# Performance work log

Hardware: AMD Instinct MI355X
Metric: run time of the kernel (lower is better)

The kernel has to match this reference:

```python
import jax, jax.numpy as jnp
import numpy as np

TAU = 0.1
NUM_HEADS = 8
HEAD_DIMS = 64


def setup_inputs() -> dict:
    key = jax.random.key(0)
    ks = jax.random.split(key, 5)
    B, T, D = 4, 1024, 512
    H, Dh = NUM_HEADS, HEAD_DIMS
    x = jax.random.normal(ks[0], (B, T, D), dtype=jnp.float32)
    scale = 1.0 / np.sqrt(D)
    wq = jax.random.normal(ks[1], (D, H * Dh), dtype=jnp.float32) * scale
    wk = jax.random.normal(ks[2], (D, H * Dh), dtype=jnp.float32) * scale
    wv = jax.random.normal(ks[3], (D, H * Dh), dtype=jnp.float32) * scale
    wo = jax.random.normal(ks[4], (H * Dh, D // H), dtype=jnp.float32) * scale
    return {"x": x, "wq": wq, "wk": wk, "wv": wv, "wo": wo}


def _scan_score(a, tau):
    # a: [B,H,T,T] soft-match scores; tau > 0 branch of _rosa_qkv_scan_score
    T = a.shape[-1]
    r = jnp.arange(T)
    future = r[:, None] < r[None, :]                       # [T,T], True above diag
    a = jnp.where(future[None, None], 0.0, a)
    # rotate columns: out[...,i,j] = a[...,i,(i+j+1) % T]
    c1 = (r[:, None] + r[None, :] + 1) % T                 # [T,T]
    a = jnp.take_along_axis(a, c1[None, None], axis=-1)
    cs = jnp.cumsum(a, axis=-2)                            # cumsum over rows i
    a = cs - jax.lax.cummax(cs * (1.0 - a), axis=2)        # run-length style scan
    # rotate back: out[...,i,j] = a[...,i,(j-i+T-1) % T]
    c2 = (r[None, :] - r[:, None] + T - 1) % T
    a = jnp.take_along_axis(a, c2[None, None], axis=-1)
    return a


def _attn_score(a, tau):
    # tau > 0 branch of _rosa_qkv_attn_score: positional tie-break + causal softmax
    T = a.shape[-1]
    r = jnp.arange(T)
    p = r.astype(a.dtype)
    pos = p[None, :] / (p[:, None] + 1.0)                  # p[i,j] = j/(i+1)
    future = r[:, None] < r[None, :]
    a = jnp.where(future[None, None], -jnp.inf, a + pos[None, None])
    return jax.nn.softmax(a / tau, axis=-1)


def reference(x, wq, wk, wv, wo):
    B, T, D = x.shape
    H, Dh = NUM_HEADS, HEAD_DIMS
    tau = TAU
    iq = (x @ wq).reshape(B, T, H, Dh)
    ik = (x @ wk).reshape(B, T, H, Dh)
    iv = (x @ wv).reshape(B, T, H, Dh)
    iq_sm = jax.nn.softmax(iq / tau, axis=-1).astype(jnp.float32)
    ik_sm = jax.nn.softmax(ik / tau, axis=-1).astype(jnp.float32)
    iv_sm = jax.nn.softmax(iv / tau, axis=-1).astype(jnp.float32)
    # match scores [B,H,T,T]
    a = jnp.einsum("bihd,bjhd->bhij", iq_sm, ik_sm)
    a = _scan_score(a, tau)
    a = _attn_score(a, tau)
    o = jnp.einsum("bhij,bjhd->bhid", a, iv_sm)            # [B,H,T,Dh]
    xv = wo.reshape(H, Dh, D // H)
    o = jnp.einsum("bhid,hde->bhie", o, xv)                # [B,H,T,D//H]
    return o.transpose(0, 2, 1, 3).reshape(B, T, D)
```

## Files before the change

### kernel.cpp

```cpp
#include <hip/hip_runtime.h>
#include <math.h>

#define BB    4
#define TT    1024
#define DD    512
#define NH    8
#define DH    64
#define BH    32
#define INV_TAU 10.0f

typedef __attribute__((ext_vector_type(8))) short short8;
typedef __attribute__((ext_vector_type(4))) float f4;
typedef __attribute__((ext_vector_type(8))) _Float16 half8;

__device__ inline unsigned short f2bf(float f) {
  unsigned u = __float_as_uint(f);
  u += 0x7FFFu + ((u >> 16) & 1u);
  return (unsigned short)(u >> 16);
}
__device__ inline float bf2f(unsigned short h) {
  return __uint_as_float(((unsigned)h) << 16);
}
__device__ inline unsigned short f2bf_t(float f) {
  return (unsigned short)(__float_as_uint(f) >> 16);
}

__global__ __launch_bounds__(256) void k_prep(
    const float* __restrict__ x, const float* __restrict__ wq,
    const float* __restrict__ wk, const float* __restrict__ wv,
    unsigned short* __restrict__ xh, unsigned short* __restrict__ xl,
    unsigned short* __restrict__ wth, unsigned short* __restrict__ wtl)
{
  __shared__ float Wf[64][65];
  const int blk = blockIdx.x;
  const int tid = threadIdx.x;
  if (blk < 2048) {
    const int i = (blk * 256 + tid) * 4;
    float4 v = *(const float4*)&x[i];
    ushort4 h, l;
    h.x = f2bf_t(v.x); l.x = f2bf_t(v.x - bf2f(h.x));
    h.y = f2bf_t(v.y); l.y = f2bf_t(v.y - bf2f(h.y));
    h.z = f2bf_t(v.z); l.z = f2bf_t(v.z - bf2f(h.z));
    h.w = f2bf_t(v.w); l.w = f2bf_t(v.w - bf2f(h.w));
    *(ushort4*)&xh[i] = h;
    *(ushort4*)&xl[i] = l;
    return;
  }
  const int b = blk - 2048;
  const int ten = b >> 6;
  const int r = b & 63;
  const int n0 = (r & 7) * 64, k0 = (r >> 3) * 64;
  const float* W = (ten == 0) ? wq : ((ten == 1) ? wk : wv);
#pragma unroll
  for (int p = 0; p < 4; ++p) {
    int kk = p * 16 + (tid >> 4);
    int nn = (tid & 15) * 4;
    float4 v = *(const float4*)&W[(size_t)(k0 + kk) * 512 + n0 + nn];
    Wf[kk][nn + 0] = v.x; Wf[kk][nn + 1] = v.y;
    Wf[kk][nn + 2] = v.z; Wf[kk][nn + 3] = v.w;
  }
  __syncthreads();
  const int n = tid >> 2, kq = tid & 3;
  size_t base = ((size_t)(ten * 512 + n0 + n)) * 512 + k0 + kq * 16;
#pragma unroll
  for (int jj = 0; jj < 4; ++jj) {
    ushort4 h, l;
    float f0 = Wf[kq * 16 + jj * 4 + 0][n];
    float f1 = Wf[kq * 16 + jj * 4 + 1][n];
    float f2 = Wf[kq * 16 + jj * 4 + 2][n];
    float f3 = Wf[kq * 16 + jj * 4 + 3][n];
    h.x = f2bf_t(f0); l.x = f2bf_t(f0 - bf2f(h.x));
    h.y = f2bf_t(f1); l.y = f2bf_t(f1 - bf2f(h.y));
    h.z = f2bf_t(f2); l.z = f2bf_t(f2 - bf2f(h.z));
    h.w = f2bf_t(f3); l.w = f2bf_t(f3 - bf2f(h.w));
    *(ushort4*)&wth[base + jj * 4] = h;
    *(ushort4*)&wtl[base + jj * 4] = l;
  }
}

__global__ __launch_bounds__(256) void k_proj_mfma(
    const unsigned short* __restrict__ xh, const unsigned short* __restrict__ xl,
    const unsigned short* __restrict__ wth, const unsigned short* __restrict__ wtl,
    unsigned short* __restrict__ qh, unsigned short* __restrict__ ql,
    unsigned short* __restrict__ kh, unsigned short* __restrict__ kl,
    float* __restrict__ vs)
{
  __shared__ unsigned short Ah[64][40];
  __shared__ unsigned short Al[64][40];
  __shared__ unsigned short Bh[128][40];
  __shared__ unsigned short Bl[128][40];
  const int tid = threadIdx.x;
  const int n0g = blockIdx.x * 128;
  const int m0 = blockIdx.y * 64;
  const int w = tid >> 6, lane = tid & 63;
  const int mw = (w & 1) * 32, nw = (w >> 1) * 64;
  const int quad = lane >> 4, l16 = lane & 15;
  const int srow = tid >> 2;
  const int sk = (tid & 3) * 8;

  f4 acc[2][4] = {};

  for (int k0 = 0; k0 < DD; k0 += 32) {
    short8 a0 = *(const short8*)&xh[(size_t)(m0 + srow) * DD + k0 + sk];
    short8 a1 = *(const short8*)&xl[(size_t)(m0 + srow) * DD + k0 + sk];
    short8 b0 = *(const short8*)&wth[(size_t)(n0g + srow) * DD + k0 + sk];
    short8 b1 = *(const short8*)&wth[(size_t)(n0g + 64 + srow) * DD + k0 + sk];
    short8 b2 = *(const short8*)&wtl[(size_t)(n0g + srow) * DD + k0 + sk];
    short8 b3 = *(const short8*)&wtl[(size_t)(n0g + 64 + srow) * DD + k0 + sk];
    *(short8*)&Ah[srow][sk] = a0;
    *(short8*)&Al[srow][sk] = a1;
    *(short8*)&Bh[srow][sk] = b0;  *(short8*)&Bh[64 + srow][sk] = b1;
    *(short8*)&Bl[srow][sk] = b2;  *(short8*)&Bl[64 + srow][sk] = b3;
    __syncthreads();

    short8 fbh[4], fbl[4];
#pragma unroll
    for (int nt = 0; nt < 4; ++nt) {
      fbh[nt] = *(const short8*)&Bh[nw + nt * 16 + l16][quad * 8];
      fbl[nt] = *(const short8*)&Bl[nw + nt * 16 + l16][quad * 8];
    }
#pragma unroll
    for (int mt = 0; mt < 2; ++mt) {
      short8 fah = *(const short8*)&Ah[mw + mt * 16 + l16][quad * 8];
      short8 fal = *(const short8*)&Al[mw + mt * 16 + l16][quad * 8];
#pragma unroll
      for (int nt = 0; nt < 4; ++nt) {
        acc[mt][nt] = __builtin_amdgcn_mfma_f32_16x16x32_bf16(fah, fbh[nt], acc[mt][nt], 0, 0, 0);
        acc[mt][nt] = __builtin_amdgcn_mfma_f32_16x16x32_bf16(fah, fbl[nt], acc[mt][nt], 0, 0, 0);
        acc[mt][nt] = __builtin_amdgcn_mfma_f32_16x16x32_bf16(fal, fbh[nt], acc[mt][nt], 0, 0, 0);
      }
    }
    __syncthreads();
  }

  const int tensor = n0g >> 9;
  const int ncol = (n0g & 511) + nw;
  const int h = ncol >> 6;
#pragma unroll
  for (int mt = 0; mt < 2; ++mt) {
#pragma unroll
    for (int r = 0; r < 4; ++r) {
      float v0 = acc[mt][0][r], v1 = acc[mt][1][r];
      float v2 = acc[mt][2][r], v3 = acc[mt][3][r];
      float mx = fmaxf(fmaxf(v0, v1), fmaxf(v2, v3));
#pragma unroll
      for (int msk = 1; msk <= 8; msk <<= 1) mx = fmaxf(mx, __shfl_xor(mx, msk, 64));
      float e0 = __expf((v0 - mx) * INV_TAU);
      float e1 = __expf((v1 - mx) * INV_TAU);
      float e2 = __expf((v2 - mx) * INV_TAU);
      float e3 = __expf((v3 - mx) * INV_TAU);
      float sm = e0 + e1 + e2 + e3;
#pragma unroll
      for (int msk = 1; msk <= 8; msk <<= 1) sm += __shfl_xor(sm, msk, 64);
      float inv = 1.0f / sm;
      int row = m0 + mw + mt * 16 + quad * 4 + r;
      int b = row >> 10, t = row & 1023;
      size_t base = (((size_t)b * NH + h) * TT + t) * DH;
      float e[4] = {e0 * inv, e1 * inv, e2 * inv, e3 * inv};
      if (tensor == 2) {
#pragma unroll
        for (int c = 0; c < 4; ++c) vs[base + l16 + c * 16] = e[c];
      } else {
        unsigned short* oh = tensor ? kh : qh;
        unsigned short* ol = tensor ? kl : ql;
#pragma unroll
        for (int c = 0; c < 4; ++c) {
          unsigned short hh = f2bf_t(e[c]);
          oh[base + l16 + c * 16] = hh;
          ol[base + l16 + c * 16] = f2bf_t(e[c] - bf2f(hh));
        }
      }
    }
  }
}

__global__ __launch_bounds__(256) void k_qkv(
    const unsigned short* __restrict__ qh, const unsigned short* __restrict__ ql,
    const unsigned short* __restrict__ kh, const unsigned short* __restrict__ kl,
    _Float16* __restrict__ A, const float* __restrict__ vs,
    unsigned short* __restrict__ vth, unsigned short* __restrict__ vtl)
{
  __shared__ char smem[4][32][68 * 2];
  const int tid = threadIdx.x;
  if (blockIdx.x >= 1088) {
    float (*Vf)[65] = (float(*)[65])smem;
    const int b = blockIdx.x - 1088;
    const int z = b & 31, t0 = (b >> 5) * 64;
#pragma unroll
    for (int it = 0; it < 4; ++it) {
      int tl = it * 16 + (tid >> 4);
      int d4 = (tid & 15) * 4;
      float4 v = *(const float4*)&vs[((size_t)z * TT + t0 + tl) * DH + d4];
      Vf[tl][d4 + 0] = v.x; Vf[tl][d4 + 1] = v.y;
      Vf[tl][d4 + 2] = v.z; Vf[tl][d4 + 3] = v.w;
    }
    __syncthreads();
#pragma unroll
    for (int it = 0; it < 8; ++it) {
      int d = it * 8 + (tid >> 5);
      int t = (tid & 31) * 2;
      float a0 = Vf[t][d], a1 = Vf[t + 1][d];
      unsigned short h0 = f2bf_t(a0), h1 = f2bf_t(a1);
      unsigned short l0 = f2bf_t(a0 - bf2f(h0)), l1 = f2bf_t(a1 - bf2f(h1));
      size_t o = ((size_t)z * DH + d) * TT + t0 + t;
      ushort2 hh; hh.x = h0; hh.y = h1;
      ushort2 ll; ll.x = l0; ll.y = l1;
      *(ushort2*)&vth[o] = hh;
      *(ushort2*)&vtl[o] = ll;
    }
    return;
  }
  const int gid = blockIdx.x * 4 + (tid >> 6);
  const int z = gid / 136;
  const int lx = gid - z * 136;
  int ti = (int)((sqrtf(8.0f * lx + 1.0f) - 1.0f) * 0.5f);
  while ((ti + 1) * (ti + 2) / 2 <= lx) ++ti;
  while (ti * (ti + 1) / 2 > lx) --ti;
  const int tj = lx - ti * (ti + 1) / 2;
  const int i0 = ti * 64, j0 = tj * 64;
  const int w = tid >> 6;
  const int lane = tid & 63;
  const int quad = lane >> 4, l16 = lane & 15;
  const size_t zb = (size_t)z * TT * DH;

  short8 fbh[4][2], fbl[4][2];
#pragma unroll
  for (int nt = 0; nt < 4; ++nt)
#pragma unroll
    for (int ks = 0; ks < 2; ++ks) {
      size_t o = zb + (size_t)(j0 + nt * 16 + l16) * DH + ks * 32 + quad * 8;
      fbh[nt][ks] = *(const short8*)&kh[o];
      fbl[nt][ks] = *(const short8*)&kl[o];
    }

  f4 acc[4][4] = {};
#pragma unroll
  for (int mt = 0; mt < 4; ++mt) {
    short8 fah[2], fal[2];
#pragma unroll
    for (int ks = 0; ks < 2; ++ks) {
      size_t o = zb + (size_t)(i0 + mt * 16 + l16) * DH + ks * 32 + quad * 8;
      fah[ks] = *(const short8*)&qh[o];
      fal[ks] = *(const short8*)&ql[o];
    }
#pragma unroll
    for (int nt = 0; nt < 4; ++nt)
#pragma unroll
      for (int ks = 0; ks < 2; ++ks) {
        acc[mt][nt] = __builtin_amdgcn_mfma_f32_16x16x32_bf16(fah[ks], fbh[nt][ks], acc[mt][nt], 0, 0, 0);
        acc[mt][nt] = __builtin_amdgcn_mfma_f32_16x16x32_bf16(fah[ks], fbl[nt][ks], acc[mt][nt], 0, 0, 0);
        acc[mt][nt] = __builtin_amdgcn_mfma_f32_16x16x32_bf16(fal[ks], fbh[nt][ks], acc[mt][nt], 0, 0, 0);
      }
  }

  _Float16* Ab = A + (size_t)z * TT * TT;
  _Float16 (*Ts)[68] = (_Float16(*)[68])smem[w];
#pragma unroll
  for (int round = 0; round < 2; ++round) {
#pragma unroll
    for (int m2 = 0; m2 < 2; ++m2) {
      int mt = round * 2 + m2;
#pragma unroll
      for (int nt = 0; nt < 4; ++nt)
#pragma unroll
        for (int r = 0; r < 4; ++r)
          Ts[m2 * 16 + quad * 4 + r][nt * 16 + l16] = (_Float16)acc[mt][nt][r];
    }
    const int rrow = lane >> 3, seg = (lane & 7) * 8;
#pragma unroll
    for (int r2 = 0; r2 < 4; ++r2) {
      int row = rrow + 8 * r2;
      half8 v = *(const half8*)&Ts[row][seg];
      *(half8*)&Ab[(size_t)(i0 + round * 32 + row) * TT + j0 + seg] = v;
    }
  }
}

__global__ __launch_bounds__(1024) void k_scan(_Float16* __restrict__ A)
{
  __shared__ float Ssum[16][64];
  __shared__ float Gmax[16][64];
  const int blk = blockIdx.x;
  const int p = blk >> 5;
  const int xb = (p < 8) ? p : (23 - p);
  const int z = blk & 31;
  const int lane = threadIdx.x & 63;
  const int w = threadIdx.x >> 6;
  _Float16* __restrict__ Ab = A + (size_t)z * TT * TT;
  const int dbase = xb * 64;
  const int d = dbase + lane;
  const int L = (TT - dbase) >> 4;
  const int r0 = dbase + w * L;

  float S = 0.0f;
#pragma unroll 8
  for (int t = 0; t < L; ++t) {
    int i = r0 + t;
    size_t idx = (i >= d) ? ((size_t)i * (TT + 1) - d) : 0;
    float s = (float)Ab[idx];
    S += (i >= d) ? s : 0.0f;
  }
  Ssum[w][lane] = S;
  __syncthreads();

  float cs_in = 0.0f;
  for (int ww = 0; ww < w; ++ww) cs_in += Ssum[ww][lane];

  {
    float lcs = 0.0f, gm = 0.0f;
#pragma unroll 8
    for (int t = 0; t < L; ++t) {
      int i = r0 + t;
      size_t idx = (i >= d) ? ((size_t)i * (TT + 1) - d) : 0;
      float s0 = (float)Ab[idx];
      float s = (i >= d) ? s0 : 0.0f;
      lcs += s;
      gm = fmaxf(gm, (cs_in + lcs) * (1.0f - s));
    }
    Gmax[w][lane] = gm;
  }
  __syncthreads();

  float m = 0.0f;
  for (int ww = 0; ww < w; ++ww) m = fmaxf(m, Gmax[ww][lane]);

  {
    float lcs = 0.0f;
#pragma unroll 8
    for (int t = 0; t < L; ++t) {
      int i = r0 + t;
      bool ok = (i >= d);
      size_t idx = ok ? ((size_t)i * (TT + 1) - d) : 0;
      float s0 = (float)Ab[idx];
      float s = ok ? s0 : 0.0f;
      lcs += s;
      float cs = cs_in + lcs;
      m = fmaxf(m, cs * (1.0f - s));
      if (ok) Ab[idx] = (_Float16)(cs - m);
    }
  }
}

__global__ __launch_bounds__(64) void k_pv(
    const _Float16* __restrict__ A, const unsigned short* __restrict__ vth,
    const unsigned short* __restrict__ vtl, float* __restrict__ oatt,
    float* __restrict__ Opart, float* __restrict__ ml)
{
  const int lane = threadIdx.x;
  const int quad = lane >> 4, l16 = lane & 15;
  const int blk = blockIdx.x;
  const int z = blk & 31;
  const int item = blk >> 5;
  int ti, band, jt0, jt1, chunk;
  bool split;
  if (item < 32) {
    ti = 8 + (item >> 2); band = item & 3; jt0 = 0; jt1 = 8; chunk = 0; split = true;
  } else {
    int i2 = item - 32;
    int l = 8 - (i2 >> 3);
    int sub = i2 & 7;
    band = sub & 3;
    if (sub < 4) { ti = l + 7; jt0 = 8; jt1 = ti + 1; chunk = 1; split = true; }
    else         { ti = l - 1; jt0 = 0; jt1 = ti + 1; chunk = 0; split = false; }
  }
  const _Float16* Az = A + (size_t)z * TT * TT;
  const unsigned short* vh = vth + (size_t)z * DH * TT;
  const unsigned short* vl = vtl + (size_t)z * DH * TT;

  const int i0 = ti * 64;
  const int irow = i0 + band * 16 + l16;
  const float invi = 1.0f / (float)(irow + 1);
  f4 acc[4] = {};
  float m_old = -3e38f, l_run = 0.0f;

  float posu[16];
#pragma unroll
  for (int u = 0; u < 16; ++u)
    posu[u] = (float)((u >> 3) * 32 + quad * 8 + (u & 7)) * invi;
  const float jstep = 64.0f * invi;
  float jtoff = (float)jt0 * jstep;

  for (int jt = jt0; jt < jt1; ++jt) {
    const bool masked = (jt == ti);
    float sc[16];
#pragma unroll
    for (int ks = 0; ks < 2; ++ks) {
      half8 hv = *(const half8*)&Az[(size_t)irow * TT + jt * 64 + ks * 32 + quad * 8];
#pragma unroll
      for (int u = 0; u < 8; ++u) sc[ks * 8 + u] = (float)hv[u];
    }
#pragma unroll
    for (int u = 0; u < 16; ++u) {
      float v = sc[u] + (jtoff + posu[u]);
      int j = jt * 64 + (u >> 3) * 32 + quad * 8 + (u & 7);
      sc[u] = (masked && j > irow) ? -3e38f : v;
    }
    float mt_ = sc[0];
#pragma unroll
    for (int u = 1; u < 16; ++u) mt_ = fmaxf(mt_, sc[u]);
    mt_ = fmaxf(mt_, __shfl_xor(mt_, 16, 64));
    mt_ = fmaxf(mt_, __shfl_xor(mt_, 32, 64));
    float m_new = fmaxf(m_old, mt_);
    float alpha = __expf((m_old - m_new) * INV_TAU);
    unsigned short ph[16], pl[16];
    float ls = 0.0f;
#pragma unroll
    for (int u = 0; u < 16; ++u) {
      float pvv = __expf((sc[u] - m_new) * INV_TAU);
      unsigned short hh = f2bf_t(pvv);
      ph[u] = hh; pl[u] = f2bf_t(pvv - bf2f(hh));
      ls += pvv;
    }
    ls += __shfl_xor(ls, 16, 64);
    ls += __shfl_xor(ls, 32, 64);
    l_run = l_run * alpha + ls;
    m_old = m_new;
#pragma unroll
    for (int rr = 0; rr < 4; ++rr) {
      float ar = __shfl(alpha, quad * 4 + rr, 64);
#pragma unroll
      for (int nt = 0; nt < 4; ++nt) acc[nt][rr] *= ar;
    }
#pragma unroll
    for (int ks = 0; ks < 2; ++ks) {
      short8 pah, pal;
#pragma unroll
      for (int u = 0; u < 8; ++u) { pah[u] = (short)ph[ks * 8 + u]; pal[u] = (short)pl[ks * 8 + u]; }
#pragma unroll
      for (int nt = 0; nt < 4; ++nt) {
        size_t vo = (size_t)(nt * 16 + l16) * TT + jt * 64 + ks * 32 + quad * 8;
        short8 fvh = *(const short8*)&vh[vo];
        short8 fvl = *(const short8*)&vl[vo];
        acc[nt] = __builtin_amdgcn_mfma_f32_16x16x32_bf16(pah, fvh, acc[nt], 0, 0, 0);
        acc[nt] = __builtin_amdgcn_mfma_f32_16x16x32_bf16(pah, fvl, acc[nt], 0, 0, 0);
        acc[nt] = __builtin_amdgcn_mfma_f32_16x16x32_bf16(pal, fvh, acc[nt], 0, 0, 0);
      }
    }
    jtoff += jstep;
  }

  if (!split) {
#pragma unroll
    for (int rr = 0; rr < 4; ++rr) {
      float lr = __shfl(l_run, quad * 4 + rr, 64);
      float inv = 1.0f / lr;
      int orow = i0 + band * 16 + quad * 4 + rr;
#pragma unroll
      for (int nt = 0; nt < 4; ++nt)
        oatt[((size_t)z * TT + orow) * DH + nt * 16 + l16] = acc[nt][rr] * inv;
    }
  } else {
    if (quad == 0) {
      int prow = i0 + band * 16 + l16 - 512;
      size_t mo = (((size_t)chunk * 32 + z) * 512 + prow) * 2;
      ml[mo + 0] = m_old;
      ml[mo + 1] = l_run;
    }
#pragma unroll
    for (int rr = 0; rr < 4; ++rr) {
      int prow = i0 + band * 16 + quad * 4 + rr - 512;
      size_t po = (((size_t)chunk * 32 + z) * 512 + prow) * 64;
#pragma unroll
      for (int nt = 0; nt < 4; ++nt)
        Opart[po + nt * 16 + l16] = acc[nt][rr];
    }
  }
}

__global__ __launch_bounds__(256) void k_oproj(
    const float* __restrict__ oatt, const float* __restrict__ wo,
    const float* __restrict__ Opart, const float* __restrict__ ml,
    float* __restrict__ out)
{
  __shared__ float Wl[64][64];
  __shared__ float Ol[16][64];
  const int z = blockIdx.y;
  const int t0 = blockIdx.x * 16;
  const int b = z >> 3, h = z & 7;
  const int tid = threadIdx.x;
  const float* wb = wo + (size_t)h * 64 * 64;
#pragma unroll
  for (int u = 0; u < 4; ++u) {
    int q = tid + 256 * u;
    int dd = q >> 4, e4 = (q & 15) * 4;
    *(float4*)&Wl[dd][e4] = *(const float4*)&wb[(size_t)dd * 64 + e4];
  }
  {
    int rr = tid >> 4, d4 = (tid & 15) * 4;
    int trow = t0 + rr;
    if (trow < 512) {
      *(float4*)&Ol[rr][d4] = *(const float4*)&oatt[((size_t)z * TT + trow) * DH + d4];
    } else {
      int pr = trow - 512;
      size_t m0o = (((size_t)0 * 32 + z) * 512 + pr) * 2;
      size_t m1o = (((size_t)1 * 32 + z) * 512 + pr) * 2;
      float m0 = ml[m0o], l0 = ml[m0o + 1];
      float m1 = ml[m1o], l1 = ml[m1o + 1];
      float mm = fmaxf(m0, m1);
      float w0 = __expf((m0 - mm) * INV_TAU);
      float w1 = __expf((m1 - mm) * INV_TAU);
      float inv = 1.0f / (l0 * w0 + l1 * w1);
      float4 o0 = *(const float4*)&Opart[(((size_t)0 * 32 + z) * 512 + pr) * 64 + d4];
      float4 o1 = *(const float4*)&Opart[(((size_t)1 * 32 + z) * 512 + pr) * 64 + d4];
      Ol[rr][d4 + 0] = (o0.x * w0 + o1.x * w1) * inv;
      Ol[rr][d4 + 1] = (o0.y * w0 + o1.y * w1) * inv;
      Ol[rr][d4 + 2] = (o0.z * w0 + o1.z * w1) * inv;
      Ol[rr][d4 + 3] = (o0.w * w0 + o1.w * w1) * inv;
    }
  }
  __syncthreads();
  const int rg = tid >> 6, e = tid & 63;
  float a0 = 0, a1 = 0, a2 = 0, a3 = 0;
#pragma unroll
  for (int dd = 0; dd < 64; ++dd) {
    float wv = Wl[dd][e];
    a0 += Ol[rg * 4 + 0][dd] * wv;
    a1 += Ol[rg * 4 + 1][dd] * wv;
    a2 += Ol[rg * 4 + 2][dd] * wv;
    a3 += Ol[rg * 4 + 3][dd] * wv;
  }
  size_t ob = ((size_t)b * TT + t0 + rg * 4) * DD + h * 64 + e;
  out[ob] = a0; out[ob + DD] = a1; out[ob + 2 * DD] = a2; out[ob + 3 * DD] = a3;
}

extern "C" void kernel_launch(void* const* d_in, const int* in_sizes, int n_in,
                              void* d_out, int out_size, void* d_ws, size_t ws_size,
                              hipStream_t stream)
{
  (void)in_sizes; (void)n_in; (void)out_size; (void)ws_size;
  const float* x  = (const float*)d_in[0];
  const float* wq = (const float*)d_in[1];
  const float* wk = (const float*)d_in[2];
  const float* wv = (const float*)d_in[3];
  const float* wo = (const float*)d_in[4];
  float* out = (float*)d_out;

  char* ws = (char*)d_ws;
  const size_t MB = 1024 * 1024;
  unsigned short* qh = (unsigned short*)(ws);
  unsigned short* ql = (unsigned short*)(ws + 4 * MB);
  unsigned short* kh = (unsigned short*)(ws + 8 * MB);
  unsigned short* kl = (unsigned short*)(ws + 12 * MB);
  float*          vs = (float*)(ws + 16 * MB);
  unsigned short* vth = (unsigned short*)(ws + 24 * MB);
  unsigned short* vtl = (unsigned short*)(ws + 28 * MB);
  float*          oatt = (float*)(ws);
  _Float16*       A  = (_Float16*)(ws + 33 * MB);
  unsigned short* xh = (unsigned short*)(ws + 33 * MB);
  unsigned short* xl = (unsigned short*)(ws + 37 * MB);
  float*          Opart = (float*)(ws + 97 * MB);
  float*          ml = (float*)(ws + 113 * MB);
  unsigned short* wth = (unsigned short*)(ws + 161 * MB);
  unsigned short* wtl = (unsigned short*)(ws + 161 * MB + 1536 * 1024);

  hipLaunchKernelGGL(k_prep, dim3(2048 + 192), dim3(256), 0, stream,
                     x, wq, wk, wv, xh, xl, wth, wtl);
  hipLaunchKernelGGL(k_proj_mfma, dim3(12, 64), dim3(256), 0, stream,
                     xh, xl, wth, wtl, qh, ql, kh, kl, vs);
  hipLaunchKernelGGL(k_qkv, dim3(1088 + 512), dim3(256), 0, stream,
                     qh, ql, kh, kl, A, vs, vth, vtl);
  hipLaunchKernelGGL(k_scan, dim3(512), dim3(1024), 0, stream, A);
  hipLaunchKernelGGL(k_pv, dim3(3072), dim3(64), 0, stream, A, vth, vtl,
                     oatt, Opart, ml);
  hipLaunchKernelGGL(k_oproj, dim3(64, 32), dim3(256), 0, stream,
                     oatt, wo, Opart, ml, out);
}
```

Measured before the change: 214.7 us.

## Split PV attention into fixed four-tile key chunks with table-driven scheduling

Rewrites the PV kernel to split every query tile's key range into chunks of up to four 64-wide tiles. A lookup table orders the work items, and the launch grows from 3072 to 5120 single-wave blocks. Each chunk does a plain two-pass softmax over its own tiles instead of an online rescale, and writes partial outputs plus max and sum. The output projection kernel then merges up to four chunks per row. The aim is better load balance and shorter critical-path blocks, at the cost of more partial-output traffic and a heavier merge step.

```diff
diff --git a/kernel.cpp b/kernel.cpp
--- a/kernel.cpp
+++ b/kernel.cpp
@@ -24,6 +24,14 @@
 __device__ inline unsigned short f2bf_t(float f) {
   return (unsigned short)(__float_as_uint(f) >> 16);
 }
+
+__device__ const unsigned char d_pvtbl[40] = {
+  12, 16, 20, 24, 28, 29, 32, 33, 36, 37, 40, 41, 44, 45, 46, 48, 49, 50,
+  52, 53, 54, 56, 57, 58, 60, 61, 62, 63,
+  8, 25, 42, 59,
+  4, 21, 38, 55,
+  0, 17, 34, 51
+};
 
 __global__ __launch_bounds__(256) void k_prep(
     const float* __restrict__ x, const float* __restrict__ wq,
@@ -343,7 +351,7 @@
 
 __global__ __launch_bounds__(64) void k_pv(
     const _Float16* __restrict__ A, const unsigned short* __restrict__ vth,
-    const unsigned short* __restrict__ vtl, float* __restrict__ oatt,
+    const unsigned short* __restrict__ vtl,
     float* __restrict__ Opart, float* __restrict__ ml)
 {
   const int lane = threadIdx.x;
@@ -351,18 +359,12 @@
   const int blk = blockIdx.x;
   const int z = blk & 31;
   const int item = blk >> 5;
-  int ti, band, jt0, jt1, chunk;
-  bool split;
-  if (item < 32) {
-    ti = 8 + (item >> 2); band = item & 3; jt0 = 0; jt1 = 8; chunk = 0; split = true;
-  } else {
-    int i2 = item - 32;
-    int l = 8 - (i2 >> 3);
-    int sub = i2 & 7;
-    band = sub & 3;
-    if (sub < 4) { ti = l + 7; jt0 = 8; jt1 = ti + 1; chunk = 1; split = true; }
-    else         { ti = l - 1; jt0 = 0; jt1 = ti + 1; chunk = 0; split = false; }
-  }
+  const int code = d_pvtbl[item >> 2];
+  const int band = item & 3;
+  const int ti = code >> 2, c = code & 3;
+  const int jt0 = c * 4;
+  const int nst = min(ti + 1 - jt0, 4);
+
   const _Float16* Az = A + (size_t)z * TT * TT;
   const unsigned short* vh = vth + (size_t)z * DH * TT;
   const unsigned short* vl = vtl + (size_t)z * DH * TT;
@@ -370,107 +372,88 @@
   const int i0 = ti * 64;
   const int irow = i0 + band * 16 + l16;
   const float invi = 1.0f / (float)(irow + 1);
-  f4 acc[4] = {};
-  float m_old = -3e38f, l_run = 0.0f;
 
   float posu[16];
 #pragma unroll
   for (int u = 0; u < 16; ++u)
     posu[u] = (float)((u >> 3) * 32 + quad * 8 + (u & 7)) * invi;
-  const float jstep = 64.0f * invi;
-  float jtoff = (float)jt0 * jstep;
-
-  for (int jt = jt0; jt < jt1; ++jt) {
-    const bool masked = (jt == ti);
-    float sc[16];
-#pragma unroll
-    for (int ks = 0; ks < 2; ++ks) {
-      half8 hv = *(const half8*)&Az[(size_t)irow * TT + jt * 64 + ks * 32 + quad * 8];
-#pragma unroll
-      for (int u = 0; u < 8; ++u) sc[ks * 8 + u] = (float)hv[u];
-    }
-#pragma unroll
-    for (int u = 0; u < 16; ++u) {
-      float v = sc[u] + (jtoff + posu[u]);
-      int j = jt * 64 + (u >> 3) * 32 + quad * 8 + (u & 7);
-      sc[u] = (masked && j > irow) ? -3e38f : v;
-    }
-    float mt_ = sc[0];
-#pragma unroll
-    for (int u = 1; u < 16; ++u) mt_ = fmaxf(mt_, sc[u]);
-    mt_ = fmaxf(mt_, __shfl_xor(mt_, 16, 64));
-    mt_ = fmaxf(mt_, __shfl_xor(mt_, 32, 64));
-    float m_new = fmaxf(m_old, mt_);
-    float alpha = __expf((m_old - m_new) * INV_TAU);
-    unsigned short ph[16], pl[16];
-    float ls = 0.0f;
-#pragma unroll
-    for (int u = 0; u < 16; ++u) {
-      float pvv = __expf((sc[u] - m_new) * INV_TAU);
-      unsigned short hh = f2bf_t(pvv);
-      ph[u] = hh; pl[u] = f2bf_t(pvv - bf2f(hh));
-      ls += pvv;
-    }
-    ls += __shfl_xor(ls, 16, 64);
-    ls += __shfl_xor(ls, 32, 64);
-    l_run = l_run * alpha + ls;
-    m_old = m_new;
-#pragma unroll
-    for (int rr = 0; rr < 4; ++rr) {
-      float ar = __shfl(alpha, quad * 4 + rr, 64);
-#pragma unroll
-      for (int nt = 0; nt < 4; ++nt) acc[nt][rr] *= ar;
-    }
-#pragma unroll
-    for (int ks = 0; ks < 2; ++ks) {
-      short8 pah, pal;
-#pragma unroll
-      for (int u = 0; u < 8; ++u) { pah[u] = (short)ph[ks * 8 + u]; pal[u] = (short)pl[ks * 8 + u]; }
-#pragma unroll
-      for (int nt = 0; nt < 4; ++nt) {
-        size_t vo = (size_t)(nt * 16 + l16) * TT + jt * 64 + ks * 32 + quad * 8;
-        short8 fvh = *(const short8*)&vh[vo];
-        short8 fvl = *(const short8*)&vl[vo];
-        acc[nt] = __builtin_amdgcn_mfma_f32_16x16x32_bf16(pah, fvh, acc[nt], 0, 0, 0);
-        acc[nt] = __builtin_amdgcn_mfma_f32_16x16x32_bf16(pah, fvl, acc[nt], 0, 0, 0);
-        acc[nt] = __builtin_amdgcn_mfma_f32_16x16x32_bf16(pal, fvh, acc[nt], 0, 0, 0);
-      }
-    }
-    jtoff += jstep;
-  }
-
-  if (!split) {
-#pragma unroll
-    for (int rr = 0; rr < 4; ++rr) {
-      float lr = __shfl(l_run, quad * 4 + rr, 64);
-      float inv = 1.0f / lr;
-      int orow = i0 + band * 16 + quad * 4 + rr;
-#pragma unroll
-      for (int nt = 0; nt < 4; ++nt)
-        oatt[((size_t)z * TT + orow) * DH + nt * 16 + l16] = acc[nt][rr] * inv;
-    }
-  } else {
-    if (quad == 0) {
-      int prow = i0 + band * 16 + l16 - 512;
-      size_t mo = (((size_t)chunk * 32 + z) * 512 + prow) * 2;
-      ml[mo + 0] = m_old;
-      ml[mo + 1] = l_run;
-    }
-#pragma unroll
-    for (int rr = 0; rr < 4; ++rr) {
-      int prow = i0 + band * 16 + quad * 4 + rr - 512;
-      size_t po = (((size_t)chunk * 32 + z) * 512 + prow) * 64;
-#pragma unroll
-      for (int nt = 0; nt < 4; ++nt)
-        Opart[po + nt * 16 + l16] = acc[nt][rr];
-    }
+
+  float sc[4][16];
+  float mx = -3e38f;
+#pragma unroll
+  for (int st = 0; st < 4; ++st) {
+    if (st < nst) {
+      const int jt = jt0 + st;
+      const bool masked = (jt == ti);
+      const float jtoff = (float)(jt * 64) * invi;
+#pragma unroll
+      for (int ks = 0; ks < 2; ++ks) {
+        half8 hv = *(const half8*)&Az[(size_t)irow * TT + jt * 64 + ks * 32 + quad * 8];
+#pragma unroll
+        for (int u = 0; u < 8; ++u) sc[st][ks * 8 + u] = (float)hv[u];
+      }
+#pragma unroll
+      for (int u = 0; u < 16; ++u) {
+        float v = sc[st][u] + (jtoff + posu[u]);
+        int j = jt * 64 + (u >> 3) * 32 + quad * 8 + (u & 7);
+        sc[st][u] = (masked && j > irow) ? -3e38f : v;
+        mx = fmaxf(mx, sc[st][u]);
+      }
+    }
+  }
+  mx = fmaxf(mx, __shfl_xor(mx, 16, 64));
+  mx = fmaxf(mx, __shfl_xor(mx, 32, 64));
+
+  f4 acc[4] = {};
+  float ls = 0.0f;
+#pragma unroll
+  for (int st = 0; st < 4; ++st) {
+    if (st < nst) {
+      const int jt = jt0 + st;
+#pragma unroll
+      for (int ks = 0; ks < 2; ++ks) {
+        short8 pah, pal;
+#pragma unroll
+        for (int u = 0; u < 8; ++u) {
+          float pvv = __expf((sc[st][ks * 8 + u] - mx) * INV_TAU);
+          ls += pvv;
+          unsigned short hh = f2bf_t(pvv);
+          pah[u] = (short)hh;
+          pal[u] = (short)f2bf_t(pvv - bf2f(hh));
+        }
+#pragma unroll
+        for (int nt = 0; nt < 4; ++nt) {
+          size_t vo = (size_t)(nt * 16 + l16) * TT + jt * 64 + ks * 32 + quad * 8;
+          short8 fvh = *(const short8*)&vh[vo];
+          short8 fvl = *(const short8*)&vl[vo];
+          acc[nt] = __builtin_amdgcn_mfma_f32_16x16x32_bf16(pah, fvh, acc[nt], 0, 0, 0);
+          acc[nt] = __builtin_amdgcn_mfma_f32_16x16x32_bf16(pah, fvl, acc[nt], 0, 0, 0);
+          acc[nt] = __builtin_amdgcn_mfma_f32_16x16x32_bf16(pal, fvh, acc[nt], 0, 0, 0);
+        }
+      }
+    }
+  }
+  ls += __shfl_xor(ls, 16, 64);
+  ls += __shfl_xor(ls, 32, 64);
+
+  if (quad == 0) {
+    size_t mo = (((size_t)c * 32 + z) * TT + irow) * 2;
+    ml[mo + 0] = mx;
+    ml[mo + 1] = ls;
+  }
+#pragma unroll
+  for (int rr = 0; rr < 4; ++rr) {
+    int orow = i0 + band * 16 + quad * 4 + rr;
+    size_t po = (((size_t)c * 32 + z) * TT + orow) * 64;
+#pragma unroll
+    for (int nt = 0; nt < 4; ++nt)
+      Opart[po + nt * 16 + l16] = acc[nt][rr];
   }
 }
 
 __global__ __launch_bounds__(256) void k_oproj(
-    const float* __restrict__ oatt, const float* __restrict__ wo,
-    const float* __restrict__ Opart, const float* __restrict__ ml,
-    float* __restrict__ out)
+    const float* __restrict__ wo, const float* __restrict__ Opart,
+    const float* __restrict__ ml, float* __restrict__ out)
 {
   __shared__ float Wl[64][64];
   __shared__ float Ol[16][64];
@@ -488,25 +471,34 @@
   {
     int rr = tid >> 4, d4 = (tid & 15) * 4;
     int trow = t0 + rr;
-    if (trow < 512) {
-      *(float4*)&Ol[rr][d4] = *(const float4*)&oatt[((size_t)z * TT + trow) * DH + d4];
-    } else {
-      int pr = trow - 512;
-      size_t m0o = (((size_t)0 * 32 + z) * 512 + pr) * 2;
-      size_t m1o = (((size_t)1 * 32 + z) * 512 + pr) * 2;
-      float m0 = ml[m0o], l0 = ml[m0o + 1];
-      float m1 = ml[m1o], l1 = ml[m1o + 1];
-      float mm = fmaxf(m0, m1);
-      float w0 = __expf((m0 - mm) * INV_TAU);
-      float w1 = __expf((m1 - mm) * INV_TAU);
-      float inv = 1.0f / (l0 * w0 + l1 * w1);
-      float4 o0 = *(const float4*)&Opart[(((size_t)0 * 32 + z) * 512 + pr) * 64 + d4];
-      float4 o1 = *(const float4*)&Opart[(((size_t)1 * 32 + z) * 512 + pr) * 64 + d4];
-      Ol[rr][d4 + 0] = (o0.x * w0 + o1.x * w1) * inv;
-      Ol[rr][d4 + 1] = (o0.y * w0 + o1.y * w1) * inv;
-      Ol[rr][d4 + 2] = (o0.z * w0 + o1.z * w1) * inv;
-      Ol[rr][d4 + 3] = (o0.w * w0 + o1.w * w1) * inv;
-    }
+    int ti = trow >> 6;
+    int nc = (ti >> 2) + 1;
+    float mv[4], lv[4];
+    float mm = -3e38f;
+#pragma unroll
+    for (int c = 0; c < 4; ++c) {
+      if (c < nc) {
+        size_t mo = (((size_t)c * 32 + z) * TT + trow) * 2;
+        mv[c] = ml[mo]; lv[c] = ml[mo + 1];
+        mm = fmaxf(mm, mv[c]);
+      }
+    }
+    float den = 0.0f;
+    float o0 = 0.0f, o1 = 0.0f, o2 = 0.0f, o3 = 0.0f;
+#pragma unroll
+    for (int c = 0; c < 4; ++c) {
+      if (c < nc) {
+        float wgt = __expf((mv[c] - mm) * INV_TAU);
+        den += lv[c] * wgt;
+        float4 oc = *(const float4*)&Opart[(((size_t)c * 32 + z) * TT + trow) * 64 + d4];
+        o0 += oc.x * wgt; o1 += oc.y * wgt; o2 += oc.z * wgt; o3 += oc.w * wgt;
+      }
+    }
+    float inv = 1.0f / den;
+    Ol[rr][d4 + 0] = o0 * inv;
+    Ol[rr][d4 + 1] = o1 * inv;
+    Ol[rr][d4 + 2] = o2 * inv;
+    Ol[rr][d4 + 3] = o3 * inv;
   }
   __syncthreads();
   const int rg = tid >> 6, e = tid & 63;
@@ -544,12 +536,11 @@
   float*          vs = (float*)(ws + 16 * MB);
   unsigned short* vth = (unsigned short*)(ws + 24 * MB);
   unsigned short* vtl = (unsigned short*)(ws + 28 * MB);
-  float*          oatt = (float*)(ws);
   _Float16*       A  = (_Float16*)(ws + 33 * MB);
   unsigned short* xh = (unsigned short*)(ws + 33 * MB);
   unsigned short* xl = (unsigned short*)(ws + 37 * MB);
   float*          Opart = (float*)(ws + 97 * MB);
-  float*          ml = (float*)(ws + 113 * MB);
+  float*          ml = (float*)(ws + 129 * MB);
   unsigned short* wth = (unsigned short*)(ws + 161 * MB);
   unsigned short* wtl = (unsigned short*)(ws + 161 * MB + 1536 * 1024);
 
@@ -560,8 +551,8 @@
   hipLaunchKernelGGL(k_qkv, dim3(1088 + 512), dim3(256), 0, stream,
                      qh, ql, kh, kl, A, vs, vth, vtl);
   hipLaunchKernelGGL(k_scan, dim3(512), dim3(1024), 0, stream, A);
-  hipLaunchKernelGGL(k_pv, dim3(3072), dim3(64), 0, stream, A, vth, vtl,
-                     oatt, Opart, ml);
+  hipLaunchKernelGGL(k_pv, dim3(5120), dim3(64), 0, stream, A, vth, vtl,
+                     Opart, ml);
   hipLaunchKernelGGL(k_oproj, dim3(64, 32), dim3(256), 0, stream,
-                     oatt, wo, Opart, ml, out);
-}
+                     wo, Opart, ml, out);
+}
```

New measurement: 216.3 us. Within noise of the previous version (+0.8%).
